# Performance work log

Measured on AMD Instinct MI355X. Metric: run time of the kernel, lower is better.

Reference implementation:

```python
import jax, jax.numpy as jnp
import numpy as np

B, T, C, H = 8, 2048, 1024, 64

def setup_inputs() -> dict:
    key = jax.random.key(0)
    k1, k2, k3, k4 = jax.random.split(key, 4)
    x = jax.random.normal(k1, (B, T, C), dtype=jnp.float32)
    sw = 1.0 / np.sqrt(C)  # Linear-like init scale
    Wq = jax.random.normal(k2, (C, H), dtype=jnp.float32) * sw
    Wk = jax.random.normal(k3, (C, H), dtype=jnp.float32) * sw
    Wv = jax.random.normal(k4, (C, H), dtype=jnp.float32) * sw
    return {"x": x, "Wq": Wq, "Wk": Wk, "Wv": Wv}

def reference(x, Wq, Wk, Wv):
    # Single-head causal self-attention (eval mode: dropout is identity).
    # Quantized GEMMs (QLinear / qmatmul) are represented by exact fp32 math.
    Bx, Tx, Cx = x.shape
    q = jnp.einsum('btc,ch->bth', x, Wq)          # [B,T,H]
    k = jnp.einsum('btc,ch->bth', x, Wk)          # [B,T,H]
    v = jnp.einsum('btc,ch->bth', x, Wv)          # [B,T,H]
    scale = k.shape[-1] ** -0.5
    wei = jnp.einsum('bth,bsh->bts', q, k) * scale  # [B,T,T]
    causal = jnp.tril(jnp.ones((Tx, Tx), dtype=bool))
    wei = jnp.where(causal, wei, -jnp.inf)
    wei = jax.nn.softmax(wei, axis=-1)
    out = jnp.einsum('bts,bsh->bth', wei, v)      # [B,T,H]
    return out
```

## Files before the change

kernel.cpp:

```cpp
#include <hip/hip_runtime.h>
#include <math.h>

#define Bz 8
#define Tz 2048
#define Cz 1024
#define Hz 64
#define BT (Bz*Tz)

typedef __attribute__((ext_vector_type(8))) short bf16x8;
typedef __attribute__((ext_vector_type(4))) float f32x4;
typedef __attribute__((ext_vector_type(4))) unsigned short us4;

#define PSTRIDE 4160

__device__ __forceinline__ unsigned short f2bf(float f) {
    union { float f; unsigned u; } v; v.f = f;
    unsigned r = v.u + 0x7fffu + ((v.u >> 16) & 1u);
    return (unsigned short)(r >> 16);
}

__device__ __forceinline__ bf16x8 pack8(const float* s) {
    bf16x8 r;
#pragma unroll
    for (int j = 0; j < 8; j++) r[j] = (short)f2bf(s[j]);
    return r;
}

__device__ __forceinline__ unsigned cvt_pk_bf16(float lo, float hi) {
    unsigned r;
    asm volatile("v_cvt_pk_bf16_f32 %0, %1, %2" : "=v"(r) : "v"(lo), "v"(hi));
    return r;
}

__device__ __forceinline__ bf16x8 cvt8(float4 a, float4 b) {
    union { unsigned u[4]; bf16x8 v; } r;
    r.u[0] = cvt_pk_bf16(a.x, a.y);
    r.u[1] = cvt_pk_bf16(a.z, a.w);
    r.u[2] = cvt_pk_bf16(b.x, b.y);
    r.u[3] = cvt_pk_bf16(b.z, b.w);
    return r.v;
}

__device__ __forceinline__ void gload16(const void* g, void* l) {
    __builtin_amdgcn_global_load_lds(
        (const __attribute__((address_space(1))) void*)g,
        (__attribute__((address_space(3))) void*)l, 16, 0, 0);
}

__global__ __launch_bounds__(256)
void wprep_kernel(const float* __restrict__ Wq, const float* __restrict__ Wk,
                  const float* __restrict__ Wv, unsigned short* __restrict__ Wti)
{
    __shared__ float T[64][65];
    const int mat = blockIdx.x >> 4;
    const int kt  = blockIdx.x & 15;
    const int k0  = kt * 64;
    const float* W = (mat == 0) ? Wq : (mat == 1) ? Wk : Wv;
    const int t  = threadIdx.x;
    const int rr = t >> 2;
    const int c4 = (t & 3) * 16;
#pragma unroll
    for (int j = 0; j < 4; j++) {
        float4 w4 = *(const float4*)&W[(size_t)(k0 + rr) * Hz + c4 + j * 4];
        T[c4 + j*4 + 0][rr] = w4.x;
        T[c4 + j*4 + 1][rr] = w4.y;
        T[c4 + j*4 + 2][rr] = w4.z;
        T[c4 + j*4 + 3][rr] = w4.w;
    }
    __syncthreads();
    const int nn  = t >> 2;
    const int sl0 = (t & 3) * 2;
    const int n   = mat * 64 + nn;
    float tmp[16];
#pragma unroll
    for (int j = 0; j < 16; j++) tmp[j] = T[nn][sl0 * 8 + j];
    unsigned short* base = &Wti[(size_t)kt * 12288 + n * 64];
    *(bf16x8*)&base[((sl0    ) ^ (n & 7)) * 8] = pack8(tmp);
    *(bf16x8*)&base[((sl0 + 1) ^ (n & 7)) * 8] = pack8(tmp + 8);
}

__global__ __launch_bounds__(512, 4)
void qkv_mfma_kernel(const float* __restrict__ x, const unsigned short* __restrict__ Wti,
                     unsigned short* __restrict__ qg, unsigned short* __restrict__ kg,
                     unsigned short* __restrict__ vT)
{
    __shared__ __align__(16) float          xsF[2][64 * 64];
    __shared__ __align__(16) unsigned short ws [2][192 * 64];

    const int t    = threadIdx.x;
    const int M0   = blockIdx.x * 64;
    const int ln   = t & 15;
    const int g    = (t & 63) >> 4;
    const int g4   = g * 4;
    const int w    = t >> 6;
    const int rg   = w & 3;
    const int wc   = w >> 2;
    const int lane = t & 63;
    const float SCq = 0.18033688011112042f;

    f32x4 acc[6];
#pragma unroll
    for (int i = 0; i < 6; i++) acc[i] = (f32x4){0.f, 0.f, 0.f, 0.f};

    auto issue = [&](int buf, int kt) {
        const int k0 = kt * 64;
#pragma unroll
        for (int j = 0; j < 2; j++) {
            const int r  = w * 8 + j * 4 + (lane >> 4);
            const int sl = (lane & 15) ^ (r & 7);
            gload16(&x[(size_t)(M0 + r) * Cz + k0 + sl * 4],
                    &xsF[buf][(w * 8 + j * 4) * 64]);
        }
#pragma unroll
        for (int j = 0; j < 3; j++) {
            const int jj = w * 3 + j;
            gload16(&Wti[(size_t)kt * 12288 + jj * 512 + lane * 8],
                    &ws[buf][jj * 512]);
        }
    };

    issue(0, 0);
    __syncthreads();
    int cur = 0;

    for (int kt = 0; kt < 16; kt++) {
        if (kt < 15) issue(cur ^ 1, kt + 1);

        bf16x8 af[2];
        const int row = rg * 16 + ln;
#pragma unroll
        for (int kc = 0; kc < 2; kc++) {
            const int s0 = kc * 8 + g * 2;
            float4 fa = *(const float4*)&xsF[cur][row * 64 + ((s0    ) ^ (row & 7)) * 4];
            float4 fb = *(const float4*)&xsF[cur][row * 64 + ((s0 + 1) ^ (row & 7)) * 4];
            af[kc] = cvt8(fa, fb);
        }
        __builtin_amdgcn_s_setprio(1);
#pragma unroll
        for (int ct = 0; ct < 6; ct++) {
            const int nn = wc * 96 + ct * 16 + ln;
#pragma unroll
            for (int kc = 0; kc < 2; kc++) {
                bf16x8 bf = *(const bf16x8*)&ws[cur][nn * 64 + ((kc*4 + g) ^ (nn & 7)) * 8];
                acc[ct] = __builtin_amdgcn_mfma_f32_16x16x32_bf16(af[kc], bf, acc[ct], 0, 0, 0);
            }
        }
        __builtin_amdgcn_s_setprio(0);
        __syncthreads();
        cur ^= 1;
    }

#pragma unroll
    for (int ct = 0; ct < 6; ct++) {
        const int col0 = wc * 96 + ct * 16;
        const int mat  = col0 >> 6;
        const int cl   = (col0 & 63) + ln;
        const int m0   = M0 + rg * 16 + g4;
        if (mat == 0) {
#pragma unroll
            for (int i = 0; i < 4; i++)
                qg[(size_t)(m0 + i) * Hz + cl] = f2bf(acc[ct][i] * SCq);
        } else if (mat == 1) {
#pragma unroll
            for (int i = 0; i < 4; i++)
                kg[(size_t)(m0 + i) * Hz + cl] = f2bf(acc[ct][i]);
        } else {
            const int b = m0 >> 11, tt = m0 & 2047;
            us4 pk;
#pragma unroll
            for (int i = 0; i < 4; i++) pk[i] = f2bf(acc[ct][i]);
            *(us4*)&vT[((size_t)b * Hz + cl) * Tz + tt] = pk;
        }
    }
}

template<int S>
__global__ __launch_bounds__(256, 4)
void attn_mfma_kernel(const unsigned short* __restrict__ qg,
                      const unsigned short* __restrict__ kg,
                      const unsigned short* __restrict__ vT,
                      float* __restrict__ pbase)
{
    __shared__ __align__(16) unsigned short Ks [2][64 * 64];
    __shared__ __align__(16) unsigned short Vts[2][64 * 64];
    __shared__ __align__(16) unsigned short Ps [4 * 16 * 64];

    const int bid = blockIdx.x;
    const int b   = bid & 7;
    const int r0  = bid >> 3;
    const int c   = r0 % S;
    const int qt  = 31 - (r0 / S);
    if (c > qt) return;
    const int q0  = qt * 64;

    const int t  = threadIdx.x;
    const int ln = t & 15;
    const int g  = (t & 63) >> 4;
    const int g4 = g * 4;
    const int w  = t >> 6;
    const int l6 = t & 63;

    const unsigned short* qb = qg + (size_t)b * Tz * Hz;
    const unsigned short* kb = kg + (size_t)b * Tz * Hz;
    const unsigned short* vb = vT + (size_t)b * Hz * Tz;

    const int rl  = l6 >> 3;
    const int swz = ((l6 & 7) ^ rl) * 8;
    auto issue_tile = [&](int buf, int s0) {
#pragma unroll
        for (int qq = 0; qq < 2; qq++) {
            const int row = w*16 + qq*8 + rl;
            gload16(&kb[(size_t)(s0 + row) * Hz + swz],
                    &Ks[buf][(w*16 + qq*8) * 64]);
            gload16(&vb[(size_t)row * Tz + s0 + swz],
                    &Vts[buf][(w*16 + qq*8) * 64]);
        }
    };

    issue_tile(0, c * 64);

    bf16x8 qf[2];
    {
        const int qrow = q0 + w*16 + ln;
        qf[0] = *(const bf16x8*)&qb[(size_t)qrow * Hz + g*8];
        qf[1] = *(const bf16x8*)&qb[(size_t)qrow * Hz + 32 + g*8];
    }

    f32x4 accO[4];
#pragma unroll
    for (int i = 0; i < 4; i++) accO[i] = (f32x4){0.f, 0.f, 0.f, 0.f};
    float lrow = 0.f;
    unsigned short* Pw = &Ps[w * 1024];
    const int pwbase = ln*64 + (g & 1) * 4;
    const int pslotx = (g >> 1);

    __syncthreads();
    int cur = 0;

    for (int s = c; s <= qt; s += S) {
        if (s + S <= qt) issue_tile(cur ^ 1, (s + S) * 64);

        const unsigned short* Kc = &Ks[cur][0];
        const unsigned short* Vc = &Vts[cur][0];

        f32x4 accS[4];
        __builtin_amdgcn_s_setprio(1);
#pragma unroll
        for (int t4 = 0; t4 < 4; t4++) {
            accS[t4] = (f32x4){0.f, 0.f, 0.f, 0.f};
#pragma unroll
            for (int kc = 0; kc < 2; kc++) {
                const int n = t4*16 + ln;
                bf16x8 kf = *(const bf16x8*)&Kc[n*64 + ((kc*4 + g) ^ (n & 7)) * 8];
                accS[t4] = __builtin_amdgcn_mfma_f32_16x16x32_bf16(kf, qf[kc], accS[t4], 0, 0, 0);
            }
        }
        __builtin_amdgcn_s_setprio(0);

        const bool diag = (s == qt);
#pragma unroll
        for (int t4 = 0; t4 < 4; t4++) {
            float pv[4];
#pragma unroll
            for (int i = 0; i < 4; i++) {
                float sv = accS[t4][i];
                if (diag && (t4*16 + g4 + i > w*16 + ln)) sv = -1e30f;
                const float p = exp2f(sv);
                lrow += p;
                pv[i] = p;
            }
            uint2 pk2;
            pk2.x = cvt_pk_bf16(pv[0], pv[1]);
            pk2.y = cvt_pk_bf16(pv[2], pv[3]);
            *(uint2*)&Pw[pwbase + ((t4*2 + pslotx) ^ (ln & 7)) * 8] = pk2;
        }

        __builtin_amdgcn_s_setprio(1);
#pragma unroll
        for (int kc = 0; kc < 2; kc++) {
            bf16x8 pa = *(const bf16x8*)&Pw[ln*64 + ((kc*4 + g) ^ (ln & 7)) * 8];
#pragma unroll
            for (int ht = 0; ht < 4; ht++) {
                const int vr2 = ht*16 + ln;
                bf16x8 vf = *(const bf16x8*)&Vc[vr2*64 + ((kc*4 + g) ^ (vr2 & 7)) * 8];
                accO[ht] = __builtin_amdgcn_mfma_f32_16x16x32_bf16(pa, vf, accO[ht], 0, 0, 0);
            }
        }
        __builtin_amdgcn_s_setprio(0);

        __syncthreads();
        cur ^= 1;
    }

    lrow += __shfl_xor(lrow, 16);
    lrow += __shfl_xor(lrow, 32);

    float* Op = pbase + (size_t)((b * 32 + qt) * S + c) * PSTRIDE;
#pragma unroll
    for (int ht = 0; ht < 4; ht++)
#pragma unroll
        for (int i = 0; i < 4; i++)
            Op[(size_t)(w*16 + g4 + i) * 64 + ht*16 + ln] = accO[ht][i];
    if (g == 0)
        Op[4096 + w*16 + ln] = lrow;
}

template<int S>
__global__ __launch_bounds__(256)
void combine_kernel(const float* __restrict__ pbase, float* __restrict__ out)
{
    const int bid = blockIdx.x;
    const int b   = bid & 7;
    const int qt  = 31 - (bid >> 3);
    const int t   = threadIdx.x;
    const int r   = t >> 2;
    const int cg  = t & 3;

    const int nch = (qt + 1 < S) ? (qt + 1) : S;
    const float* P0 = pbase + (size_t)(b * 32 + qt) * S * PSTRIDE;

    float denom = 0.f;
    float4 o[4];
#pragma unroll
    for (int j = 0; j < 4; j++) o[j] = make_float4(0.f, 0.f, 0.f, 0.f);
    for (int cc = 0; cc < nch; cc++) {
        const float* Pc = P0 + (size_t)cc * PSTRIDE;
        denom += Pc[4096 + r];
#pragma unroll
        for (int j = 0; j < 4; j++) {
            float4 v4 = *(const float4*)&Pc[(size_t)r * 64 + cg * 16 + j * 4];
            o[j].x += v4.x; o[j].y += v4.y; o[j].z += v4.z; o[j].w += v4.w;
        }
    }
    const float inv = 1.f / denom;
    float* ob = out + ((size_t)b * Tz + qt * 64 + r) * Hz + cg * 16;
#pragma unroll
    for (int j = 0; j < 4; j++)
        *(float4*)&ob[j * 4] = make_float4(o[j].x * inv, o[j].y * inv,
                                           o[j].z * inv, o[j].w * inv);
}

extern "C" void kernel_launch(void* const* d_in, const int* in_sizes, int n_in,
                              void* d_out, int out_size, void* d_ws, size_t ws_size,
                              hipStream_t stream) {
    const float* x  = (const float*)d_in[0];
    const float* Wq = (const float*)d_in[1];
    const float* Wk = (const float*)d_in[2];
    const float* Wv = (const float*)d_in[3];

    unsigned short* Wti = (unsigned short*)d_ws;
    unsigned short* qg  = Wti + 196608;
    unsigned short* kg  = qg + (size_t)BT * Hz;
    unsigned short* vT  = kg + (size_t)BT * Hz;
    const size_t baseShorts = 196608 + 3 * (size_t)BT * Hz;
    float* pbase = (float*)((char*)d_ws + baseShorts * 2);
    float* out = (float*)d_out;

    wprep_kernel<<<48, 256, 0, stream>>>(Wq, Wk, Wv, Wti);
    qkv_mfma_kernel<<<BT / 64, 512, 0, stream>>>(x, Wti, qg, kg, vT);

    const size_t base = baseShorts * 2;
    const size_t per  = (size_t)8 * 32 * PSTRIDE * 4;
    if (ws_size >= base + 4 * per) {
        attn_mfma_kernel<4><<<8 * 32 * 4, 256, 0, stream>>>(qg, kg, vT, pbase);
        combine_kernel<4><<<256, 256, 0, stream>>>(pbase, out);
    } else {
        attn_mfma_kernel<1><<<8 * 32 * 1, 256, 0, stream>>>(qg, kg, vT, pbase);
        combine_kernel<1><<<256, 256, 0, stream>>>(pbase, out);
    }
}
```

Before: 52.32 us.

## Triple-buffer QKV projection loads with explicit vmcnt waits and barriers

Replaces the double-buffered x/W tile pipeline in the QKV MFMA kernel with a three-stage ring buffer. Loads are issued two tiles ahead, and vmcnt waits are counted explicitly so that more global-to-LDS traffic is in flight during the MFMA work. The change uses 1.5x the shared memory and drops the min-blocks-per-CU launch bound, which may lower occupancy. It also adds a second barrier per iteration.

```diff
diff --git a/kernel.cpp b/kernel.cpp
--- a/kernel.cpp
+++ b/kernel.cpp
@@ -79,13 +79,13 @@
     *(bf16x8*)&base[((sl0 + 1) ^ (n & 7)) * 8] = pack8(tmp + 8);
 }
 
-__global__ __launch_bounds__(512, 4)
+__global__ __launch_bounds__(512)
 void qkv_mfma_kernel(const float* __restrict__ x, const unsigned short* __restrict__ Wti,
                      unsigned short* __restrict__ qg, unsigned short* __restrict__ kg,
                      unsigned short* __restrict__ vT)
 {
-    __shared__ __align__(16) float          xsF[2][64 * 64];
-    __shared__ __align__(16) unsigned short ws [2][192 * 64];
+    __shared__ __align__(16) float          xsF[3][64 * 64];
+    __shared__ __align__(16) unsigned short ws [3][192 * 64];
 
     const int t    = threadIdx.x;
     const int M0   = blockIdx.x * 64;
@@ -119,20 +119,21 @@
         }
     };
 
-    issue(0, 0);
-    __syncthreads();
-    int cur = 0;
-
-    for (int kt = 0; kt < 16; kt++) {
-        if (kt < 15) issue(cur ^ 1, kt + 1);
-
+    issue(0, 0); issue(1, 1); issue(2, 2);
+    asm volatile("s_waitcnt vmcnt(10)" ::: "memory");
+    __builtin_amdgcn_sched_barrier(0);
+    __builtin_amdgcn_s_barrier();
+    __builtin_amdgcn_sched_barrier(0);
+
+    int bufR = 0;
+    for (int kt = 0; kt < 16; ++kt) {
         bf16x8 af[2];
         const int row = rg * 16 + ln;
 #pragma unroll
         for (int kc = 0; kc < 2; kc++) {
             const int s0 = kc * 8 + g * 2;
-            float4 fa = *(const float4*)&xsF[cur][row * 64 + ((s0    ) ^ (row & 7)) * 4];
-            float4 fb = *(const float4*)&xsF[cur][row * 64 + ((s0 + 1) ^ (row & 7)) * 4];
+            float4 fa = *(const float4*)&xsF[bufR][row * 64 + ((s0    ) ^ (row & 7)) * 4];
+            float4 fb = *(const float4*)&xsF[bufR][row * 64 + ((s0 + 1) ^ (row & 7)) * 4];
             af[kc] = cvt8(fa, fb);
         }
         __builtin_amdgcn_s_setprio(1);
@@ -141,13 +142,31 @@
             const int nn = wc * 96 + ct * 16 + ln;
 #pragma unroll
             for (int kc = 0; kc < 2; kc++) {
-                bf16x8 bf = *(const bf16x8*)&ws[cur][nn * 64 + ((kc*4 + g) ^ (nn & 7)) * 8];
+                bf16x8 bf = *(const bf16x8*)&ws[bufR][nn * 64 + ((kc*4 + g) ^ (nn & 7)) * 8];
                 acc[ct] = __builtin_amdgcn_mfma_f32_16x16x32_bf16(af[kc], bf, acc[ct], 0, 0, 0);
             }
         }
         __builtin_amdgcn_s_setprio(0);
-        __syncthreads();
-        cur ^= 1;
+
+        if (kt == 15) break;
+
+        __builtin_amdgcn_sched_barrier(0);
+        __builtin_amdgcn_s_barrier();
+        __builtin_amdgcn_sched_barrier(0);
+
+        if (kt < 13) {
+            issue(bufR, kt + 3);
+            asm volatile("s_waitcnt vmcnt(10)" ::: "memory");
+        } else if (kt == 13) {
+            asm volatile("s_waitcnt vmcnt(5)" ::: "memory");
+        } else {
+            asm volatile("s_waitcnt vmcnt(0)" ::: "memory");
+        }
+        __builtin_amdgcn_sched_barrier(0);
+        __builtin_amdgcn_s_barrier();
+        __builtin_amdgcn_sched_barrier(0);
+
+        bufR = (bufR == 2) ? 0 : bufR + 1;
     }
 
 #pragma unroll
```

Result: no change. 51.71 us (-1.2%).
